# Optimization experiments

Hardware: AMD Instinct MI355X
Metric: run time of the kernel (lower is better)

## Reference

```python
import jax, jax.numpy as jnp
import numpy as np

N_NODES = 100000
N_EDGES = 1600000
N_GRAPHS = 256
D_IN = 128
D_HID = 128
D_OUT = 64


def graph_conv(x, src, dst, W_rel, b_rel, W_root):
    # PyG GraphConv: out = lin_rel(mean_{j->i} x_j) + lin_root(x)
    msgs = jax.ops.segment_sum(x[src], dst, num_segments=N_NODES)  # [N, d]
    deg = jax.ops.segment_sum(jnp.ones((src.shape[0],), x.dtype), dst, num_segments=N_NODES)
    agg = msgs / jnp.maximum(deg, 1.0)[:, None]
    return agg @ W_rel + b_rel + x @ W_root


def setup_inputs() -> dict:
    key = jax.random.key(0)
    ks = jax.random.split(key, 12)
    x = jax.random.normal(ks[0], (N_NODES, D_IN), dtype=jnp.float32)
    edge_index = jax.random.randint(ks[1], (2, N_EDGES), 0, N_NODES, dtype=jnp.int64)
    batch = jnp.sort(jax.random.randint(ks[2], (N_NODES,), 0, N_GRAPHS, dtype=jnp.int64))
    def lin(k, fan_in, fan_out):
        bound = 1.0 / np.sqrt(fan_in)
        return jax.random.uniform(k, (fan_in, fan_out), jnp.float32, -bound, bound)
    inp = {
        "x": x, "edge_index": edge_index, "batch": batch,
        "W1_rel": lin(ks[3], D_IN, D_HID), "b1_rel": jnp.zeros((D_HID,), jnp.float32), "W1_root": lin(ks[4], D_IN, D_HID),
        "W2_rel": lin(ks[5], D_HID, D_HID), "b2_rel": jnp.zeros((D_HID,), jnp.float32), "W2_root": lin(ks[6], D_HID, D_HID),
        "W3_rel": lin(ks[7], D_HID, D_HID), "b3_rel": jnp.zeros((D_HID,), jnp.float32), "W3_root": lin(ks[8], D_HID, D_HID),
        "Wl": lin(ks[9], D_HID, D_OUT), "bl": jnp.zeros((D_OUT,), jnp.float32),
    }
    return inp


def reference(x, edge_index, batch, W1_rel, b1_rel, W1_root, W2_rel, b2_rel, W2_root,
              W3_rel, b3_rel, W3_root, Wl, bl):
    src, dst = edge_index[0], edge_index[1]
    h = jax.nn.relu(graph_conv(x, src, dst, W1_rel, b1_rel, W1_root))
    h = jax.nn.relu(graph_conv(h, src, dst, W2_rel, b2_rel, W2_root))
    h = graph_conv(h, src, dst, W3_rel, b3_rel, W3_root)
    # global mean pool over graphs
    sums = jax.ops.segment_sum(h, batch, num_segments=N_GRAPHS)          # [G, d]
    cnts = jax.ops.segment_sum(jnp.ones((h.shape[0],), h.dtype), batch, num_segments=N_GRAPHS)
    pooled = sums / jnp.maximum(cnts, 1.0)[:, None]
    # dropout is identity at inference
    return pooled @ Wl + bl  # [G, D_OUT]
```

## Files before the change

kernel.cpp:

```cpp
#include <hip/hip_runtime.h>
#include <hip/hip_bf16.h>

#define N_NODES  100000
#define N_EDGES  1600000
#define N_GRAPHS 256
#define DCH      128
#define DOUT     64
#define SCAN_TILE 2048
#define POOL_CHUNK 128
#define NB       391
#define PADB     512
#define SLACK    4608
#define CHUNK    4096

typedef short v8s __attribute__((ext_vector_type(8)));
typedef float v4f __attribute__((ext_vector_type(4)));

static __device__ __forceinline__ float bf2f(unsigned short u) {
    unsigned int x = ((unsigned int)u) << 16;
    return __builtin_bit_cast(float, x);
}
static __device__ __forceinline__ unsigned short f2bf(float f) {
    unsigned int x = __builtin_bit_cast(unsigned int, f);
    unsigned int r = (x + 0x7fffu + ((x >> 16) & 1u)) >> 16;
    return (unsigned short)r;
}
static __device__ __forceinline__ int clampi(int v, int lo, int hi) {
    return v < lo ? lo : (v > hi ? hi : v);
}

__global__ void cvt_kernel(const float* __restrict__ in, unsigned short* __restrict__ out) {
    size_t i = ((size_t)blockIdx.x * blockDim.x + threadIdx.x) * 4;
    if (i + 3 < (size_t)N_NODES * DCH) {
        float4 f = *reinterpret_cast<const float4*>(in + i);
        uint2 o;
        o.x = ((unsigned)f2bf(f.y) << 16) | (unsigned)f2bf(f.x);
        o.y = ((unsigned)f2bf(f.w) << 16) | (unsigned)f2bf(f.z);
        *reinterpret_cast<uint2*>(out + i) = o;
    }
}

__global__ void initcur_kernel(int* __restrict__ gcur) {
    int b = blockIdx.x * blockDim.x + threadIdx.x;
    if (b < PADB) gcur[b] = b * SLACK;
}

__global__ void __launch_bounds__(256) binA_kernel(const int* __restrict__ src, const int* __restrict__ dst,
                                                   int* __restrict__ gcur, uint2* __restrict__ region) {
    __shared__ uint2 stage[CHUNK];
    __shared__ int hcnt[PADB], hcnt2[PADB], hoff[PADB], garr[PADB];
    __shared__ int s2[256];
    int tid = threadIdx.x;
    int e0  = blockIdx.x * CHUNK;
    int nedge = N_EDGES - e0; if (nedge > CHUNK) nedge = CHUNK;

    for (int b = tid; b < PADB; b += 256) { hcnt[b] = 0; hcnt2[b] = 0; }
    __syncthreads();

    int es[16], ed[16];
    #pragma unroll
    for (int j = 0; j < 16; j++) {
        int e = e0 + j * 256 + tid;
        if (e < N_EDGES) {
            es[j] = clampi(src[e], 0, N_NODES - 1);
            ed[j] = clampi(dst[e], 0, N_NODES - 1);
            atomicAdd(&hcnt[ed[j] >> 8], 1);
        } else { es[j] = -1; ed[j] = 0; }
    }
    __syncthreads();

    int v0 = hcnt[2 * tid], v1 = hcnt[2 * tid + 1];
    s2[tid] = v0 + v1; __syncthreads();
    for (int off = 1; off < 256; off <<= 1) {
        int x = (tid >= off) ? s2[tid - off] : 0;
        __syncthreads();
        s2[tid] += x;
        __syncthreads();
    }
    int excl = s2[tid] - (v0 + v1);
    hoff[2 * tid] = excl; hoff[2 * tid + 1] = excl + v0;
    __syncthreads();

    for (int b = tid; b < NB; b += 256) {
        int c = hcnt[b];
        garr[b] = (c > 0) ? atomicAdd(&gcur[b], c) : 0;
    }
    __syncthreads();

    #pragma unroll
    for (int j = 0; j < 16; j++) {
        if (es[j] >= 0) {
            int b = ed[j] >> 8;
            int pos = atomicAdd(&hcnt2[b], 1) + hoff[b];
            stage[pos] = (uint2){(unsigned)es[j], (unsigned)ed[j]};
        }
    }
    __syncthreads();

    for (int i = tid; i < nedge; i += 256) {
        uint2 en = stage[i];
        int b = (int)(en.y >> 8);
        int gpos = garr[b] + (i - hoff[b]);
        if (gpos < (b + 1) * SLACK) region[gpos] = en;
    }
}

__global__ void __launch_bounds__(256) binCount_kernel(const uint2* __restrict__ region, const int* __restrict__ gcur,
                                                       int* __restrict__ cnt) {
    __shared__ int h[256];
    int b = blockIdx.x, tid = threadIdx.x;
    h[tid] = 0; __syncthreads();
    int size = gcur[b] - b * SLACK;
    if (size > SLACK) size = SLACK;
    int node0 = b * 256;
    for (int j = tid; j < size; j += 256) {
        unsigned loc = region[b * SLACK + j].y - (unsigned)node0;
        if (loc < 256u) atomicAdd(&h[loc], 1);
    }
    __syncthreads();
    int node = node0 + tid;
    if (node < N_NODES) cnt[node] = h[tid];
}

__global__ void scanA(const int* __restrict__ cnt, int* __restrict__ bsum) {
    __shared__ int sdata[256];
    int t = threadIdx.x;
    int base = blockIdx.x * SCAN_TILE + t * 8;
    int s = 0;
    #pragma unroll
    for (int j = 0; j < 8; j++) { int i = base + j; s += (i < N_NODES) ? cnt[i] : 0; }
    sdata[t] = s; __syncthreads();
    for (int off = 128; off > 0; off >>= 1) {
        if (t < off) sdata[t] += sdata[t + off];
        __syncthreads();
    }
    if (t == 0) bsum[blockIdx.x] = sdata[0];
}

__global__ void scanB(const int* __restrict__ bsum, int* __restrict__ bbase, int nblocks) {
    if (threadIdx.x == 0) {
        int run = 0;
        for (int i = 0; i < nblocks; i++) { bbase[i] = run; run += bsum[i]; }
        bbase[nblocks] = run;
    }
}

__global__ void scanC(const int* __restrict__ cnt, const int* __restrict__ bbase,
                      int* __restrict__ rowptr, int nblocks) {
    __shared__ int sdata[256];
    int t = threadIdx.x;
    int base = blockIdx.x * SCAN_TILE + t * 8;
    int v[8]; int s = 0;
    #pragma unroll
    for (int j = 0; j < 8; j++) { int i = base + j; v[j] = (i < N_NODES) ? cnt[i] : 0; s += v[j]; }
    sdata[t] = s; __syncthreads();
    for (int off = 1; off < 256; off <<= 1) {
        int x = (t >= off) ? sdata[t - off] : 0;
        __syncthreads();
        sdata[t] += x;
        __syncthreads();
    }
    int excl = sdata[t] - s + bbase[blockIdx.x];
    #pragma unroll
    for (int j = 0; j < 8; j++) {
        int i = base + j;
        if (i < N_NODES) rowptr[i] = excl;
        excl += v[j];
    }
    if (blockIdx.x == 0 && t == 0) rowptr[N_NODES] = bbase[nblocks];
}

__global__ void __launch_bounds__(256) binB_kernel(const uint2* __restrict__ region, const int* __restrict__ gcur,
                                                   const int* __restrict__ rowptr, int* __restrict__ csr) {
    __shared__ int cur[256];
    int b   = blockIdx.x;
    int tid = threadIdx.x;
    int node0 = b * 256;
    int nmax  = N_NODES - node0; if (nmax > 256) nmax = 256;
    if (tid < nmax) cur[tid] = rowptr[node0 + tid];
    __syncthreads();
    int size = gcur[b] - b * SLACK;
    if (size > SLACK) size = SLACK;
    for (int j = tid; j < size; j += 256) {
        uint2 en = region[b * SLACK + j];
        unsigned loc = en.y - (unsigned)node0;
        if (loc < 256u) {
            int p = atomicAdd(&cur[loc], 1);
            if (p >= 0 && p < N_EDGES) csr[p] = (int)en.x;
        }
    }
}

__global__ void wfrag_kernel(const float* __restrict__ W1rel, const float* __restrict__ W1root,
                             const float* __restrict__ W2rel, const float* __restrict__ W2root,
                             const float* __restrict__ W3rel, const float* __restrict__ W3root,
                             unsigned short* __restrict__ frag) {
    int gid = blockIdx.x * blockDim.x + threadIdx.x;
    if (gid >= 3 * 8 * 8 * 64) return;
    int lane = gid & 63;
    int nt   = (gid >> 6) & 7;
    int kt   = (gid >> 9) & 7;
    int L    = gid >> 12;
    const float* rel  = (L == 0) ? W1rel  : (L == 1) ? W2rel  : W3rel;
    const float* root = (L == 0) ? W1root : (L == 1) ? W2root : W3root;
    int n  = nt * 16 + (lane & 15);
    int k0 = kt * 32 + (lane >> 4) * 8;
    unsigned short o[8];
    #pragma unroll
    for (int j = 0; j < 8; j++) {
        int k = k0 + j;
        float w = (k < 128) ? rel[k * 128 + n] : root[(k - 128) * 128 + n];
        o[j] = f2bf(w);
    }
    uint4 u;
    u.x = (unsigned)o[0] | ((unsigned)o[1] << 16);
    u.y = (unsigned)o[2] | ((unsigned)o[3] << 16);
    u.z = (unsigned)o[4] | ((unsigned)o[5] << 16);
    u.w = (unsigned)o[6] | ((unsigned)o[7] << 16);
    *reinterpret_cast<uint4*>(frag + (size_t)gid * 8) = u;
}

__global__ void agg_kernel(const unsigned short* __restrict__ hin, const int* __restrict__ rowptr,
                           const int* __restrict__ csr, unsigned short* __restrict__ agg) {
    int wave = threadIdx.x >> 6;
    int lane = threadIdx.x & 63;
    int node = blockIdx.x * 4 + wave;
    if (node >= N_NODES) return;
    int r0 = rowptr[node], r1 = rowptr[node + 1];
    int l16 = lane & 15;
    float a0 = 0.f, a1 = 0.f;
    for (int c = r0; c < r1; c += 16) {
        int m = r1 - c; if (m > 16) m = 16;
        int idx = csr[c + (l16 < m ? l16 : 0)];
        #pragma unroll
        for (int j = 0; j < 16; j++) {
            int s = __shfl(idx, j);
            unsigned int v = *reinterpret_cast<const unsigned int*>(hin + (size_t)s * DCH + lane * 2);
            float w = (j < m) ? 1.0f : 0.0f;
            a0 = fmaf(w, bf2f((unsigned short)(v & 0xffffu)), a0);
            a1 = fmaf(w, bf2f((unsigned short)(v >> 16)), a1);
        }
    }
    int deg = r1 - r0;
    float inv = 1.0f / (float)(deg > 1 ? deg : 1);
    a0 *= inv; a1 *= inv;
    unsigned int o = ((unsigned int)f2bf(a1) << 16) | (unsigned int)f2bf(a0);
    *reinterpret_cast<unsigned int*>(agg + (size_t)node * DCH + lane * 2) = o;
}

__global__ void gemm_kernel(const unsigned short* agg, const unsigned short* __restrict__ root,
                            const unsigned short* __restrict__ frag, const float* __restrict__ bias,
                            unsigned short* hout, int relu) {
    int wave = threadIdx.x >> 6;
    int lane = threadIdx.x & 63;
    int quad = lane >> 4;
    int ml   = lane & 15;
    int base = blockIdx.x * 128 + wave * 32;
    int r0 = clampi(base + ml, 0, N_NODES - 1);
    int r1 = clampi(base + 16 + ml, 0, N_NODES - 1);
    v4f acc[2][8];
    #pragma unroll
    for (int h = 0; h < 2; h++)
        #pragma unroll
        for (int nt = 0; nt < 8; nt++) acc[h][nt] = (v4f){0.f, 0.f, 0.f, 0.f};
    #pragma unroll
    for (int kt = 0; kt < 8; kt++) {
        const unsigned short* asrc = (kt < 4) ? agg : root;
        int ak = (kt & 3) * 32 + quad * 8;
        v8s a0 = *reinterpret_cast<const v8s*>(asrc + (size_t)r0 * DCH + ak);
        v8s a1 = *reinterpret_cast<const v8s*>(asrc + (size_t)r1 * DCH + ak);
        #pragma unroll
        for (int nt = 0; nt < 8; nt++) {
            v8s b = *reinterpret_cast<const v8s*>(frag + (((size_t)(kt * 8 + nt)) * 64 + lane) * 8);
            acc[0][nt] = __builtin_amdgcn_mfma_f32_16x16x32_bf16(a0, b, acc[0][nt], 0, 0, 0);
            acc[1][nt] = __builtin_amdgcn_mfma_f32_16x16x32_bf16(a1, b, acc[1][nt], 0, 0, 0);
        }
    }
    #pragma unroll
    for (int h = 0; h < 2; h++) {
        int mbase = base + h * 16 + quad * 4;
        #pragma unroll
        for (int nt = 0; nt < 8; nt++) {
            int n = nt * 16 + ml;
            float bv = bias[n];
            #pragma unroll
            for (int r = 0; r < 4; r++) {
                int row = mbase + r;
                if (row < N_NODES) {
                    float v = acc[h][nt][r] + bv;
                    if (relu) v = fmaxf(v, 0.f);
                    hout[(size_t)row * DCH + n] = f2bf(v);
                }
            }
        }
    }
}

__global__ void pool_kernel(const unsigned short* __restrict__ h, const int* __restrict__ batch,
                            float* __restrict__ psum, int* __restrict__ pcnt) {
    int c  = threadIdx.x;
    int n0 = blockIdx.x * POOL_CHUNK;
    int n1 = n0 + POOL_CHUNK < N_NODES ? n0 + POOL_CHUNK : N_NODES;
    if (n0 >= n1) return;
    int cur = clampi(batch[n0], 0, N_GRAPHS - 1);
    float acc = 0.f;
    int run = 0;
    for (int n = n0; n < n1; n++) {
        int g = clampi(batch[n], 0, N_GRAPHS - 1);
        if (g != cur) {
            atomicAdd(&psum[cur * DCH + c], acc);
            if (c == 0) atomicAdd(&pcnt[cur], run);
            acc = 0.f; run = 0; cur = g;
        }
        acc += bf2f(h[(size_t)n * DCH + c]);
        run++;
    }
    atomicAdd(&psum[cur * DCH + c], acc);
    if (c == 0) atomicAdd(&pcnt[cur], run);
}

__global__ void final_kernel(const float* __restrict__ psum, const int* __restrict__ pcnt,
                             const float* __restrict__ Wl, const float* __restrict__ bl,
                             float* __restrict__ out) {
    int g = blockIdx.x;
    int o = threadIdx.x;
    int c_ = pcnt[g];
    float inv = 1.0f / (float)(c_ > 1 ? c_ : 1);
    float acc = 0.f;
    for (int c = 0; c < DCH; c++) {
        acc += psum[g * DCH + c] * Wl[c * DOUT + o];
    }
    out[g * DOUT + o] = acc * inv + bl[o];
}

extern "C" void kernel_launch(void* const* d_in, const int* in_sizes, int n_in,
                              void* d_out, int out_size, void* d_ws, size_t ws_size,
                              hipStream_t stream) {
    const float* x     = (const float*)d_in[0];
    const int*   edge  = (const int*)d_in[1];
    const int*   src   = edge;
    const int*   dst   = edge + N_EDGES;
    const int*   batch = (const int*)d_in[2];
    const float* W1rel  = (const float*)d_in[3];
    const float* b1     = (const float*)d_in[4];
    const float* W1root = (const float*)d_in[5];
    const float* W2rel  = (const float*)d_in[6];
    const float* b2     = (const float*)d_in[7];
    const float* W2root = (const float*)d_in[8];
    const float* W3rel  = (const float*)d_in[9];
    const float* b3     = (const float*)d_in[10];
    const float* W3root = (const float*)d_in[11];
    const float* Wl     = (const float*)d_in[12];
    const float* bl     = (const float*)d_in[13];
    float* out = (float*)d_out;

    char* ws = (char*)d_ws;
    size_t off = 0;
    auto carve = [&](size_t bytes) -> void* {
        void* p = ws + off;
        off += (bytes + 255) & ~(size_t)255;
        return p;
    };
    int*            cnt    = (int*)carve((size_t)N_NODES * 4);
    int*            rowptr = (int*)carve((size_t)(N_NODES + 1) * 4);
    int*            csr    = (int*)carve((size_t)N_EDGES * 4);
    int*            bsum   = (int*)carve(64 * 4);
    int*            bbase  = (int*)carve(65 * 4);
    int*            gcur   = (int*)carve((size_t)PADB * 4);
    unsigned short* frag   = (unsigned short*)carve((size_t)3 * 8 * 8 * 64 * 8 * 2);
    unsigned short* B1     = (unsigned short*)carve((size_t)N_NODES * DCH * 2);
    unsigned short* B2     = (unsigned short*)carve((size_t)N_NODES * DCH * 2);
    float*          psum   = (float*)carve((size_t)N_GRAPHS * DCH * 4);
    int*            pcnt   = (int*)carve((size_t)N_GRAPHS * 4);
    uint2*          region = (uint2*)B1;

    hipMemsetAsync(psum, 0, (size_t)N_GRAPHS * DCH * 4, stream);
    hipMemsetAsync(pcnt, 0, (size_t)N_GRAPHS * 4, stream);

    initcur_kernel<<<2, 256, 0, stream>>>(gcur);
    binA_kernel<<<(N_EDGES + CHUNK - 1) / CHUNK, 256, 0, stream>>>(src, dst, gcur, region);
    binCount_kernel<<<NB, 256, 0, stream>>>(region, gcur, cnt);
    int nblocks = (N_NODES + SCAN_TILE - 1) / SCAN_TILE;
    scanA<<<nblocks, 256, 0, stream>>>(cnt, bsum);
    scanB<<<1, 64, 0, stream>>>(bsum, bbase, nblocks);
    scanC<<<nblocks, 256, 0, stream>>>(cnt, bbase, rowptr, nblocks);
    binB_kernel<<<NB, 256, 0, stream>>>(region, gcur, rowptr, csr);
    cvt_kernel<<<(N_NODES * DCH / 4 + 255) / 256, 256, 0, stream>>>(x, B2);
    wfrag_kernel<<<(3 * 8 * 8 * 64 + 255) / 256, 256, 0, stream>>>(W1rel, W1root, W2rel, W2root, W3rel, W3root, frag);

    const int aggGrid  = (N_NODES + 3) / 4;
    const int gemmGrid = (N_NODES + 127) / 128;

    agg_kernel<<<aggGrid, 256, 0, stream>>>(B2, rowptr, csr, B1);
    gemm_kernel<<<gemmGrid, 256, 0, stream>>>(B1, B2, frag, b1, B1, 1);
    agg_kernel<<<aggGrid, 256, 0, stream>>>(B1, rowptr, csr, B2);
    gemm_kernel<<<gemmGrid, 256, 0, stream>>>(B2, B1, frag + 32768, b2, B2, 1);
    agg_kernel<<<aggGrid, 256, 0, stream>>>(B2, rowptr, csr, B1);
    gemm_kernel<<<gemmGrid, 256, 0, stream>>>(B1, B2, frag + 65536, b3, B1, 0);

    pool_kernel<<<(N_NODES + POOL_CHUNK - 1) / POOL_CHUNK, 128, 0, stream>>>(B1, batch, psum, pcnt);
    final_kernel<<<N_GRAPHS, DOUT, 0, stream>>>(psum, pcnt, Wl, bl, out);
}
```

Baseline: 473.1 us.

## Fuse CSR scan into bucket scan and binCount; fuse pooling with final linear

Replaces the three-kernel node-count scan with a single-block scan over per-bucket edge counts, followed by a per-bucket local scan inside binCount that writes rowptr directly. The gcur init kernel becomes a memset, with the slack offset added in binA instead. Pooling and the final linear layer are merged into one per-graph kernel. That kernel finds each graph's node range by binary search on the sorted batch array, which removes the atomics and the psum/pcnt memsets. The aim is fewer launches and less global traffic, at the cost of serial per-graph pooling with only 256 blocks and a reliance on batch being sorted.

```diff
diff --git a/kernel.cpp b/kernel.cpp
--- a/kernel.cpp
+++ b/kernel.cpp
@@ -6,7 +6,6 @@
 #define N_GRAPHS 256
 #define DCH      128
 #define DOUT     64
-#define SCAN_TILE 2048
 #define POOL_CHUNK 128
 #define NB       391
 #define PADB     512
@@ -40,11 +39,6 @@
     }
 }
 
-__global__ void initcur_kernel(int* __restrict__ gcur) {
-    int b = blockIdx.x * blockDim.x + threadIdx.x;
-    if (b < PADB) gcur[b] = b * SLACK;
-}
-
 __global__ void __launch_bounds__(256) binA_kernel(const int* __restrict__ src, const int* __restrict__ dst,
                                                    int* __restrict__ gcur, uint2* __restrict__ region) {
     __shared__ uint2 stage[CHUNK];
@@ -83,7 +77,7 @@
 
     for (int b = tid; b < NB; b += 256) {
         int c = hcnt[b];
-        garr[b] = (c > 0) ? atomicAdd(&gcur[b], c) : 0;
+        garr[b] = b * SLACK + ((c > 0) ? atomicAdd(&gcur[b], c) : 0);
     }
     __syncthreads();
 
@@ -105,69 +99,45 @@
     }
 }
 
+__global__ void bucketScan_kernel(const int* __restrict__ gcur, int* __restrict__ rowptrBase,
+                                  int* __restrict__ rowptr) {
+    __shared__ int s[512];
+    int t = threadIdx.x;
+    int c = 0;
+    if (t < NB) { c = gcur[t]; if (c > SLACK) c = SLACK; }
+    s[t] = c; __syncthreads();
+    for (int off = 1; off < 512; off <<= 1) {
+        int x = (t >= off) ? s[t - off] : 0;
+        __syncthreads();
+        s[t] += x;
+        __syncthreads();
+    }
+    rowptrBase[t] = s[t] - c;
+    if (t == 511) rowptr[N_NODES] = s[511];
+}
+
 __global__ void __launch_bounds__(256) binCount_kernel(const uint2* __restrict__ region, const int* __restrict__ gcur,
-                                                       int* __restrict__ cnt) {
+                                                       const int* __restrict__ rowptrBase, int* __restrict__ rowptr) {
     __shared__ int h[256];
+    __shared__ int sc[256];
     int b = blockIdx.x, tid = threadIdx.x;
     h[tid] = 0; __syncthreads();
-    int size = gcur[b] - b * SLACK;
-    if (size > SLACK) size = SLACK;
+    int size = gcur[b]; if (size > SLACK) size = SLACK;
     int node0 = b * 256;
     for (int j = tid; j < size; j += 256) {
         unsigned loc = region[b * SLACK + j].y - (unsigned)node0;
         if (loc < 256u) atomicAdd(&h[loc], 1);
     }
     __syncthreads();
+    int v = h[tid]; sc[tid] = v; __syncthreads();
+    for (int off = 1; off < 256; off <<= 1) {
+        int x = (tid >= off) ? sc[tid - off] : 0;
+        __syncthreads();
+        sc[tid] += x;
+        __syncthreads();
+    }
     int node = node0 + tid;
-    if (node < N_NODES) cnt[node] = h[tid];
-}
-
-__global__ void scanA(const int* __restrict__ cnt, int* __restrict__ bsum) {
-    __shared__ int sdata[256];
-    int t = threadIdx.x;
-    int base = blockIdx.x * SCAN_TILE + t * 8;
-    int s = 0;
-    #pragma unroll
-    for (int j = 0; j < 8; j++) { int i = base + j; s += (i < N_NODES) ? cnt[i] : 0; }
-    sdata[t] = s; __syncthreads();
-    for (int off = 128; off > 0; off >>= 1) {
-        if (t < off) sdata[t] += sdata[t + off];
-        __syncthreads();
-    }
-    if (t == 0) bsum[blockIdx.x] = sdata[0];
-}
-
-__global__ void scanB(const int* __restrict__ bsum, int* __restrict__ bbase, int nblocks) {
-    if (threadIdx.x == 0) {
-        int run = 0;
-        for (int i = 0; i < nblocks; i++) { bbase[i] = run; run += bsum[i]; }
-        bbase[nblocks] = run;
-    }
-}
-
-__global__ void scanC(const int* __restrict__ cnt, const int* __restrict__ bbase,
-                      int* __restrict__ rowptr, int nblocks) {
-    __shared__ int sdata[256];
-    int t = threadIdx.x;
-    int base = blockIdx.x * SCAN_TILE + t * 8;
-    int v[8]; int s = 0;
-    #pragma unroll
-    for (int j = 0; j < 8; j++) { int i = base + j; v[j] = (i < N_NODES) ? cnt[i] : 0; s += v[j]; }
-    sdata[t] = s; __syncthreads();
-    for (int off = 1; off < 256; off <<= 1) {
-        int x = (t >= off) ? sdata[t - off] : 0;
-        __syncthreads();
-        sdata[t] += x;
-        __syncthreads();
-    }
-    int excl = sdata[t] - s + bbase[blockIdx.x];
-    #pragma unroll
-    for (int j = 0; j < 8; j++) {
-        int i = base + j;
-        if (i < N_NODES) rowptr[i] = excl;
-        excl += v[j];
-    }
-    if (blockIdx.x == 0 && t == 0) rowptr[N_NODES] = bbase[nblocks];
+    if (node < N_NODES) rowptr[node] = rowptrBase[b] + sc[tid] - v;
 }
 
 __global__ void __launch_bounds__(256) binB_kernel(const uint2* __restrict__ region, const int* __restrict__ gcur,
@@ -179,8 +149,7 @@
     int nmax  = N_NODES - node0; if (nmax > 256) nmax = 256;
     if (tid < nmax) cur[tid] = rowptr[node0 + tid];
     __syncthreads();
-    int size = gcur[b] - b * SLACK;
-    if (size > SLACK) size = SLACK;
+    int size = gcur[b]; if (size > SLACK) size = SLACK;
     for (int j = tid; j < size; j += 256) {
         uint2 en = region[b * SLACK + j];
         unsigned loc = en.y - (unsigned)node0;
@@ -296,41 +265,37 @@
     }
 }
 
-__global__ void pool_kernel(const unsigned short* __restrict__ h, const int* __restrict__ batch,
-                            float* __restrict__ psum, int* __restrict__ pcnt) {
-    int c  = threadIdx.x;
-    int n0 = blockIdx.x * POOL_CHUNK;
-    int n1 = n0 + POOL_CHUNK < N_NODES ? n0 + POOL_CHUNK : N_NODES;
-    if (n0 >= n1) return;
-    int cur = clampi(batch[n0], 0, N_GRAPHS - 1);
+static __device__ __forceinline__ int lowerb(const int* __restrict__ a, int n, int key) {
+    int lo = 0, hi = n;
+    while (lo < hi) { int mid = (lo + hi) >> 1; if (a[mid] < key) lo = mid + 1; else hi = mid; }
+    return lo;
+}
+
+__global__ void __launch_bounds__(128) poolfinal_kernel(const unsigned short* __restrict__ h,
+                                                        const int* __restrict__ batch,
+                                                        const float* __restrict__ Wl, const float* __restrict__ bl,
+                                                        float* __restrict__ out) {
+    __shared__ float ps[DCH];
+    __shared__ int bounds[2];
+    int g = blockIdx.x, tid = threadIdx.x;
+    if (tid == 0) {
+        bounds[0] = lowerb(batch, N_NODES, g);
+        bounds[1] = lowerb(batch, N_NODES, g + 1);
+    }
+    __syncthreads();
+    int lo = bounds[0], hi = bounds[1];
     float acc = 0.f;
-    int run = 0;
-    for (int n = n0; n < n1; n++) {
-        int g = clampi(batch[n], 0, N_GRAPHS - 1);
-        if (g != cur) {
-            atomicAdd(&psum[cur * DCH + c], acc);
-            if (c == 0) atomicAdd(&pcnt[cur], run);
-            acc = 0.f; run = 0; cur = g;
-        }
-        acc += bf2f(h[(size_t)n * DCH + c]);
-        run++;
-    }
-    atomicAdd(&psum[cur * DCH + c], acc);
-    if (c == 0) atomicAdd(&pcnt[cur], run);
-}
-
-__global__ void final_kernel(const float* __restrict__ psum, const int* __restrict__ pcnt,
-                             const float* __restrict__ Wl, const float* __restrict__ bl,
-                             float* __restrict__ out) {
-    int g = blockIdx.x;
-    int o = threadIdx.x;
-    int c_ = pcnt[g];
-    float inv = 1.0f / (float)(c_ > 1 ? c_ : 1);
-    float acc = 0.f;
-    for (int c = 0; c < DCH; c++) {
-        acc += psum[g * DCH + c] * Wl[c * DOUT + o];
-    }
-    out[g * DOUT + o] = acc * inv + bl[o];
+    for (int n = lo; n < hi; n++) acc += bf2f(h[(size_t)n * DCH + tid]);
+    int cnt = hi - lo;
+    float inv = 1.0f / (float)(cnt > 1 ? cnt : 1);
+    ps[tid] = acc * inv;
+    __syncthreads();
+    if (tid < DOUT) {
+        float o = 0.f;
+        #pragma unroll 4
+        for (int c = 0; c < DCH; c++) o += ps[c] * Wl[c * DOUT + tid];
+        out[g * DOUT + tid] = o + bl[tid];
+    }
 }
 
 extern "C" void kernel_launch(void* const* d_in, const int* in_sizes, int n_in,
@@ -361,29 +326,20 @@
         off += (bytes + 255) & ~(size_t)255;
         return p;
     };
-    int*            cnt    = (int*)carve((size_t)N_NODES * 4);
-    int*            rowptr = (int*)carve((size_t)(N_NODES + 1) * 4);
-    int*            csr    = (int*)carve((size_t)N_EDGES * 4);
-    int*            bsum   = (int*)carve(64 * 4);
-    int*            bbase  = (int*)carve(65 * 4);
-    int*            gcur   = (int*)carve((size_t)PADB * 4);
-    unsigned short* frag   = (unsigned short*)carve((size_t)3 * 8 * 8 * 64 * 8 * 2);
-    unsigned short* B1     = (unsigned short*)carve((size_t)N_NODES * DCH * 2);
-    unsigned short* B2     = (unsigned short*)carve((size_t)N_NODES * DCH * 2);
-    float*          psum   = (float*)carve((size_t)N_GRAPHS * DCH * 4);
-    int*            pcnt   = (int*)carve((size_t)N_GRAPHS * 4);
-    uint2*          region = (uint2*)B1;
-
-    hipMemsetAsync(psum, 0, (size_t)N_GRAPHS * DCH * 4, stream);
-    hipMemsetAsync(pcnt, 0, (size_t)N_GRAPHS * 4, stream);
-
-    initcur_kernel<<<2, 256, 0, stream>>>(gcur);
+    int*            rowptr  = (int*)carve((size_t)(N_NODES + 1) * 4);
+    int*            csr     = (int*)carve((size_t)N_EDGES * 4);
+    int*            gcur    = (int*)carve((size_t)PADB * 4);
+    int*            rpbase  = (int*)carve((size_t)(PADB + 1) * 4);
+    unsigned short* frag    = (unsigned short*)carve((size_t)3 * 8 * 8 * 64 * 8 * 2);
+    unsigned short* B1      = (unsigned short*)carve((size_t)N_NODES * DCH * 2);
+    unsigned short* B2      = (unsigned short*)carve((size_t)N_NODES * DCH * 2);
+    uint2*          region  = (uint2*)B1;
+
+    hipMemsetAsync(gcur, 0, (size_t)PADB * 4, stream);
+
     binA_kernel<<<(N_EDGES + CHUNK - 1) / CHUNK, 256, 0, stream>>>(src, dst, gcur, region);
-    binCount_kernel<<<NB, 256, 0, stream>>>(region, gcur, cnt);
-    int nblocks = (N_NODES + SCAN_TILE - 1) / SCAN_TILE;
-    scanA<<<nblocks, 256, 0, stream>>>(cnt, bsum);
-    scanB<<<1, 64, 0, stream>>>(bsum, bbase, nblocks);
-    scanC<<<nblocks, 256, 0, stream>>>(cnt, bbase, rowptr, nblocks);
+    bucketScan_kernel<<<1, 512, 0, stream>>>(gcur, rpbase, rowptr);
+    binCount_kernel<<<NB, 256, 0, stream>>>(region, gcur, rpbase, rowptr);
     binB_kernel<<<NB, 256, 0, stream>>>(region, gcur, rowptr, csr);
     cvt_kernel<<<(N_NODES * DCH / 4 + 255) / 256, 256, 0, stream>>>(x, B2);
     wfrag_kernel<<<(3 * 8 * 8 * 64 + 255) / 256, 256, 0, stream>>>(W1rel, W1root, W2rel, W2root, W3rel, W3root, frag);
@@ -398,6 +354,5 @@
     agg_kernel<<<aggGrid, 256, 0, stream>>>(B2, rowptr, csr, B1);
     gemm_kernel<<<gemmGrid, 256, 0, stream>>>(B1, B2, frag + 65536, b3, B1, 0);
 
-    pool_kernel<<<(N_NODES + POOL_CHUNK - 1) / POOL_CHUNK, 128, 0, stream>>>(B1, batch, psum, pcnt);
-    final_kernel<<<N_GRAPHS, DOUT, 0, stream>>>(psum, pcnt, Wl, bl, out);
-}
+    poolfinal_kernel<<<N_GRAPHS, 128, 0, stream>>>(B1, batch, Wl, bl, out);
+}
```

Result: slower. 525.0 us (+11.0%).
